# Kernel tuning notes

Hardware: AMD Instinct MI355X
Metric: run time of the kernel (lower is better)

The kernel has to match this reference:

```python
import jax, jax.numpy as jnp
import numpy as np


def setup_inputs() -> dict:
    key = jax.random.key(0)
    k1, k2 = jax.random.split(key)
    x = jax.random.normal(k1, (32, 64, 64, 64), dtype=jnp.float32)  # [B, C, H, W]
    limit = 3 ** 0.5
    embeddings = jax.random.uniform(k2, (64, 512), dtype=jnp.float32,
                                    minval=-limit, maxval=limit)  # [D, K]
    return {"x": x, "embeddings": embeddings}


def reference(x, embeddings):
    B, D, H, W = x.shape
    # NCHW -> NHWC -> [N, D]
    flat_x = jnp.transpose(x, (0, 2, 3, 1)).reshape(-1, D)
    distances = (
        jnp.sum(flat_x ** 2, axis=1, keepdims=True)
        - 2.0 * flat_x @ embeddings
        + jnp.sum(embeddings ** 2, axis=0, keepdims=True)
    )
    encoding_indices = jnp.argmin(distances, axis=1)  # [N]
    # gather codebook rows: embeddings.T is [K, D]
    quantized = embeddings.T[encoding_indices].reshape(B, H, W, D)
    quantized = jnp.transpose(quantized, (0, 3, 1, 2))  # back to NCHW
    commitment_loss = jnp.mean((x - jax.lax.stop_gradient(quantized)) ** 2)
    # straight-through estimator
    quantized_ste = x + jax.lax.stop_gradient(quantized - x)
    return quantized_ste, commitment_loss, encoding_indices.reshape(B, -1)
```

## Files before the change

kernel.cpp:

```cpp
#include <hip/hip_runtime.h>

#define D      64
#define K      512
#define Q_OFF  0
#define L_OFF  8388608
#define I_OFF  8388609

#define WS_ET    0
#define WS_EN    32768
#define WS_ENH   33280
#define WS_PART  33792
#define WS_BH    40960
#define WS_BL    57344

#define SEL_SCALE 16384.0f
#define SEL_BIAS  (160.0f * 16384.0f)

typedef __attribute__((ext_vector_type(8))) short short8;
typedef __attribute__((ext_vector_type(4))) float f32x4;

static __device__ __forceinline__ unsigned short f2bf(float f) {
    unsigned u = __float_as_uint(f);
    u += 0x7fffu + ((u >> 16) & 1u);
    return (unsigned short)(u >> 16);
}
static __device__ __forceinline__ float bf2f(unsigned short h) {
    return __uint_as_float(((unsigned)h) << 16);
}

__device__ __forceinline__ void gload_lds16(const float* g, float* l) {
    __builtin_amdgcn_global_load_lds(
        (const __attribute__((address_space(1))) unsigned int*)g,
        (__attribute__((address_space(3))) unsigned int*)l, 16, 0, 0);
}

__global__ __launch_bounds__(256) void vq_prep(const float* __restrict__ E,
                                               float* __restrict__ ws) {
    int g = blockIdx.x * 256 + threadIdx.x;
    int t = g >> 6, lane = g & 63;
    int col = lane & 15, kg = lane >> 4;
    int code = t * 16 + col;
    short8* bhp = (short8*)(ws + WS_BH);
    short8* blp = (short8*)(ws + WS_BL);
#pragma unroll
    for (int s = 0; s < 2; ++s) {
        short8 h, l;
#pragma unroll
        for (int j = 0; j < 8; ++j) {
            int k = s * 32 + kg * 8 + j;
            float v = -E[k * K + code];
            unsigned short hb = f2bf(v);
            h[j] = (short)hb;
            l[j] = (short)f2bf(v - bf2f(hb));
        }
        bhp[(t * 2 + s) * 64 + lane] = h;
        blp[(t * 2 + s) * 64 + lane] = l;
    }
    if (g < K) {
        float nsq = 0.f;
#pragma unroll 8
        for (int d = 0; d < D; ++d) {
            float v = E[d * K + g];
            ws[WS_ET + g * D + d] = v;
            nsq = fmaf(v, v, nsq);
        }
        ws[WS_EN + g]  = nsq;
        ws[WS_ENH + g] = 0.5f * nsq;
    }
}

__device__ __forceinline__ float dot16(const float* __restrict__ er,
                                       const float* __restrict__ xv) {
    const float4* e4 = (const float4*)er;
    float a0 = 0.f, a1 = 0.f, a2 = 0.f, a3 = 0.f;
#pragma unroll
    for (int q = 0; q < 4; ++q) {
        float4 e = e4[q];
        a0 = fmaf(xv[4*q+0], e.x, a0);
        a1 = fmaf(xv[4*q+1], e.y, a1);
        a2 = fmaf(xv[4*q+2], e.z, a2);
        a3 = fmaf(xv[4*q+3], e.w, a3);
    }
    return (a0 + a1) + (a2 + a3);
}

__global__ __launch_bounds__(128, 8) void vq_fused(const float* __restrict__ x,
                                                   float* __restrict__ ws,
                                                   float* __restrict__ out,
                                                   float* __restrict__ partial) {
    __shared__ float sbuf[2][1024];
    __shared__ unsigned sc[32];
    __shared__ float2 sdot[4][32];
    __shared__ float wsum[2];

    const int tid = threadIdx.x, w = tid >> 6, lane = tid & 63;
    const int col = lane & 15, rowg = lane >> 4;
    const int pixw = blockIdx.x * 32 + w * 16;

    const float* bh    = ws + WS_BH;
    const float* bl    = ws + WS_BL;
    const float* enh_g = ws + WS_ENH;

    gload_lds16(bh + tid * 4, sbuf[0] + tid * 4);
    gload_lds16(bl + tid * 4, sbuf[0] + 512 + tid * 4);

    short8 ah[2], al[2];
    {
        int pix = pixw + col;
        const float* xp = x + ((size_t)(pix >> 12) << 18) + (pix & 4095);
#pragma unroll
        for (int s = 0; s < 2; ++s) {
            short8 h, l;
#pragma unroll
            for (int j = 0; j < 8; ++j) {
                float v = xp[(size_t)(s * 32 + rowg * 8 + j) << 12];
                unsigned short hb = f2bf(v);
                h[j] = (short)hb;
                l[j] = (short)f2bf(v - bf2f(hb));
            }
            ah[s] = h; al[s] = l;
        }
    }

    unsigned m1[4], m2[4];
#pragma unroll
    for (int r = 0; r < 4; ++r) { m1[r] = 0xFFFFFFFFu; m2[r] = 0xFFFFFFFFu; }

    __syncthreads();

    for (int c = 0; c < 32; ++c) {
        if (c + 1 < 32) {
            const float* sh = bh + (c + 1) * 512;
            const float* sl = bl + (c + 1) * 512;
            float* db = sbuf[(c + 1) & 1];
            gload_lds16(sh + tid * 4, db + tid * 4);
            gload_lds16(sl + tid * 4, db + 512 + tid * 4);
        }

        const short8* sb = (const short8*)sbuf[c & 1];
        const float ev = enh_g[c * 16 + col];
        const unsigned codev = (unsigned)(c * 16 + col);

        short8 cbh0 = sb[lane];
        short8 cbh1 = sb[64 + lane];
        short8 cbl0 = sb[128 + lane];
        short8 cbl1 = sb[192 + lane];

        f32x4 acc = { ev, ev, ev, ev };
        __builtin_amdgcn_s_setprio(1);
        acc = __builtin_amdgcn_mfma_f32_16x16x32_bf16(ah[0], cbh0, acc, 0, 0, 0);
        acc = __builtin_amdgcn_mfma_f32_16x16x32_bf16(al[0], cbh0, acc, 0, 0, 0);
        acc = __builtin_amdgcn_mfma_f32_16x16x32_bf16(ah[0], cbl0, acc, 0, 0, 0);
        acc = __builtin_amdgcn_mfma_f32_16x16x32_bf16(ah[1], cbh1, acc, 0, 0, 0);
        acc = __builtin_amdgcn_mfma_f32_16x16x32_bf16(al[1], cbh1, acc, 0, 0, 0);
        acc = __builtin_amdgcn_mfma_f32_16x16x32_bf16(ah[1], cbl1, acc, 0, 0, 0);
        __builtin_amdgcn_s_setprio(0);

#pragma unroll
        for (int r = 0; r < 4; ++r) {
            unsigned p0 = (((unsigned)fmaf(acc[r], SEL_SCALE, SEL_BIAS)) << 9) + codev;
            m2[r] = min(m2[r], max(m1[r], p0));
            m1[r] = min(m1[r], p0);
        }

        __syncthreads();
    }

#pragma unroll
    for (int r = 0; r < 4; ++r) {
        unsigned v1 = m1[r], v2 = m2[r];
#pragma unroll
        for (int m = 1; m < 16; m <<= 1) {
            unsigned o1 = (unsigned)__shfl_xor((int)v1, m, 16);
            unsigned o2 = (unsigned)__shfl_xor((int)v2, m, 16);
            v2 = min(max(v1, o1), min(v2, o2));
            v1 = min(v1, o1);
        }
        if (col == r)
            sc[w * 16 + rowg * 4 + r] = (v1 & 511u) | ((v2 & 511u) << 16);
    }
    __syncthreads();

    const float* ET = ws + WS_ET;
    const float* EN = ws + WS_EN;
    const int pl   = tid & 31;
    const int part = tid >> 5;
    const int n    = blockIdx.x * 32 + pl;
    const int b    = n >> 12;
    const int hw   = n & 4095;

    unsigned pk = sc[pl];
    int c1 = (int)(pk & 0xffffu), c2 = (int)(pk >> 16);

    const float* xp2 = x + ((size_t)b << 18) + ((size_t)part << 16) + hw;
    float xv2[16];
#pragma unroll
    for (int d = 0; d < 16; ++d) xv2[d] = xp2[(size_t)d << 12];

    float dp1 = dot16(ET + (c1 << 6) + part * 16, xv2);
    float dp2 = dot16(ET + (c2 << 6) + part * 16, xv2);
    sdot[part][pl] = make_float2(dp1, dp2);
    __syncthreads();
    float2 q0 = sdot[0][pl], q1 = sdot[1][pl], q2 = sdot[2][pl], q3 = sdot[3][pl];
    float d1 = fmaf(-2.f, (q0.x + q1.x) + (q2.x + q3.x), EN[c1]);
    float d2 = fmaf(-2.f, (q0.y + q1.y) + (q2.y + q3.y), EN[c2]);
    bool sw = (d2 < d1) || (d2 == d1 && c2 < c1);
    int bestk = sw ? c2 : c1;

    if (part == 0) out[I_OFF + n] = (float)bestk;

    const float* qv = ET + (bestk << 6) + part * 16;
    float* op = out + Q_OFF + ((size_t)b << 18) + ((size_t)part << 16) + hw;
    float lsum = 0.f;
#pragma unroll
    for (int d = 0; d < 16; ++d) {
        float qd = qv[d];
        op[(size_t)d << 12] = qd;
        float diff = xv2[d] - qd;
        lsum = fmaf(diff, diff, lsum);
    }

#pragma unroll
    for (int off = 32; off > 0; off >>= 1)
        lsum += __shfl_down(lsum, off, 64);
    if ((tid & 63) == 0) wsum[tid >> 6] = lsum;
    __syncthreads();
    if (tid == 0)
        partial[blockIdx.x] = wsum[0] + wsum[1];
}

__global__ __launch_bounds__(256) void vq_final(const float* __restrict__ partial,
                                                float* __restrict__ out) {
    int t = threadIdx.x;
    float s = 0.f;
#pragma unroll
    for (int i = 0; i < 16; ++i) s += partial[t + 256 * i];
#pragma unroll
    for (int off = 32; off > 0; off >>= 1)
        s += __shfl_down(s, off, 64);
    __shared__ float wsum[4];
    if ((t & 63) == 0) wsum[t >> 6] = s;
    __syncthreads();
    if (t == 0)
        out[L_OFF] = ((wsum[0] + wsum[1]) + (wsum[2] + wsum[3])) * (1.f / 8388608.f);
}

extern "C" void kernel_launch(void* const* d_in, const int* in_sizes, int n_in,
                              void* d_out, int out_size, void* d_ws, size_t ws_size,
                              hipStream_t stream) {
    const float* x = (const float*)d_in[0];
    const float* E = (const float*)d_in[1];
    float* out = (float*)d_out;
    float* ws  = (float*)d_ws;

    hipLaunchKernelGGL(vq_prep,  dim3(8),    dim3(256), 0, stream, E, ws);
    hipLaunchKernelGGL(vq_fused, dim3(4096), dim3(128), 0, stream, x, ws, out, ws + WS_PART);
    hipLaunchKernelGGL(vq_final, dim3(1),    dim3(256), 0, stream, ws + WS_PART, out);
}
```

Before: 61.64 us.

## Keep codebook slices register-resident per wave and loop over pixel tiles

Each of the 8 waves in a 512-thread block now holds a fixed 64-code slice of the bf16 hi/lo codebook in registers. Every wave loops over 16 pixel tiles and computes top-2 candidates for its slice, and the per-slice candidates are merged through shared memory. This removes the per-iteration LDS streaming of the codebook and the block barriers inside the main loop, but each wave now re-reads and re-splits x for every tile, so x is loaded eight times. The grid shrinks to 512 blocks, which lowers occupancy and parallelism, and the final reduction is adjusted to match.

```diff
diff --git a/kernel.cpp b/kernel.cpp
--- a/kernel.cpp
+++ b/kernel.cpp
@@ -26,12 +26,6 @@
 }
 static __device__ __forceinline__ float bf2f(unsigned short h) {
     return __uint_as_float(((unsigned)h) << 16);
-}
-
-__device__ __forceinline__ void gload_lds16(const float* g, float* l) {
-    __builtin_amdgcn_global_load_lds(
-        (const __attribute__((address_space(1))) unsigned int*)g,
-        (__attribute__((address_space(3))) unsigned int*)l, 16, 0, 0);
 }
 
 __global__ __launch_bounds__(256) void vq_prep(const float* __restrict__ E,
@@ -84,157 +78,160 @@
     return (a0 + a1) + (a2 + a3);
 }
 
-__global__ __launch_bounds__(128, 8) void vq_fused(const float* __restrict__ x,
+__global__ __launch_bounds__(512, 2) void vq_fused(const float* __restrict__ x,
                                                    float* __restrict__ ws,
                                                    float* __restrict__ out,
                                                    float* __restrict__ partial) {
-    __shared__ float sbuf[2][1024];
-    __shared__ unsigned sc[32];
-    __shared__ float2 sdot[4][32];
-    __shared__ float wsum[2];
+    __shared__ uint2  scand[16 * 16 * 9];
+    __shared__ float2 sdot[4][128];
+    __shared__ float  wsum8[8];
 
     const int tid = threadIdx.x, w = tid >> 6, lane = tid & 63;
     const int col = lane & 15, rowg = lane >> 4;
-    const int pixw = blockIdx.x * 32 + w * 16;
-
-    const float* bh    = ws + WS_BH;
-    const float* bl    = ws + WS_BL;
-    const float* enh_g = ws + WS_ENH;
-
-    gload_lds16(bh + tid * 4, sbuf[0] + tid * 4);
-    gload_lds16(bl + tid * 4, sbuf[0] + 512 + tid * 4);
-
-    short8 ah[2], al[2];
-    {
-        int pix = pixw + col;
-        const float* xp = x + ((size_t)(pix >> 12) << 18) + (pix & 4095);
+
+    const short8* bhp = (const short8*)(ws + WS_BH);
+    const short8* blp = (const short8*)(ws + WS_BL);
+
+    short8 Bh[4][2], Bl[4][2];
+#pragma unroll
+    for (int nt = 0; nt < 4; ++nt)
 #pragma unroll
         for (int s = 0; s < 2; ++s) {
-            short8 h, l;
-#pragma unroll
-            for (int j = 0; j < 8; ++j) {
-                float v = xp[(size_t)(s * 32 + rowg * 8 + j) << 12];
-                unsigned short hb = f2bf(v);
-                h[j] = (short)hb;
-                l[j] = (short)f2bf(v - bf2f(hb));
+            int t = 4 * w + nt;
+            Bh[nt][s] = bhp[(t * 2 + s) * 64 + lane];
+            Bl[nt][s] = blp[(t * 2 + s) * 64 + lane];
+        }
+    float evc[4]; unsigned codev[4];
+#pragma unroll
+    for (int nt = 0; nt < 4; ++nt) {
+        evc[nt]   = ws[WS_ENH + (4 * w + nt) * 16 + col];
+        codev[nt] = (unsigned)((4 * w + nt) * 16 + col);
+    }
+
+    for (int m = 0; m < 16; ++m) {
+        const int pixw = (blockIdx.x * 16 + m) * 16;
+
+        short8 ah[2], al[2];
+        {
+            int pix = pixw + col;
+            const float* xp = x + ((size_t)(pix >> 12) << 18) + (pix & 4095);
+#pragma unroll
+            for (int s = 0; s < 2; ++s) {
+                short8 h, l;
+#pragma unroll
+                for (int j = 0; j < 8; ++j) {
+                    float v = xp[(size_t)(s * 32 + rowg * 8 + j) << 12];
+                    unsigned short hb = f2bf(v);
+                    h[j] = (short)hb;
+                    l[j] = (short)f2bf(v - bf2f(hb));
+                }
+                ah[s] = h; al[s] = l;
             }
-            ah[s] = h; al[s] = l;
-        }
-    }
-
-    unsigned m1[4], m2[4];
-#pragma unroll
-    for (int r = 0; r < 4; ++r) { m1[r] = 0xFFFFFFFFu; m2[r] = 0xFFFFFFFFu; }
-
-    __syncthreads();
-
-    for (int c = 0; c < 32; ++c) {
-        if (c + 1 < 32) {
-            const float* sh = bh + (c + 1) * 512;
-            const float* sl = bl + (c + 1) * 512;
-            float* db = sbuf[(c + 1) & 1];
-            gload_lds16(sh + tid * 4, db + tid * 4);
-            gload_lds16(sl + tid * 4, db + 512 + tid * 4);
-        }
-
-        const short8* sb = (const short8*)sbuf[c & 1];
-        const float ev = enh_g[c * 16 + col];
-        const unsigned codev = (unsigned)(c * 16 + col);
-
-        short8 cbh0 = sb[lane];
-        short8 cbh1 = sb[64 + lane];
-        short8 cbl0 = sb[128 + lane];
-        short8 cbl1 = sb[192 + lane];
-
-        f32x4 acc = { ev, ev, ev, ev };
-        __builtin_amdgcn_s_setprio(1);
-        acc = __builtin_amdgcn_mfma_f32_16x16x32_bf16(ah[0], cbh0, acc, 0, 0, 0);
-        acc = __builtin_amdgcn_mfma_f32_16x16x32_bf16(al[0], cbh0, acc, 0, 0, 0);
-        acc = __builtin_amdgcn_mfma_f32_16x16x32_bf16(ah[0], cbl0, acc, 0, 0, 0);
-        acc = __builtin_amdgcn_mfma_f32_16x16x32_bf16(ah[1], cbh1, acc, 0, 0, 0);
-        acc = __builtin_amdgcn_mfma_f32_16x16x32_bf16(al[1], cbh1, acc, 0, 0, 0);
-        acc = __builtin_amdgcn_mfma_f32_16x16x32_bf16(ah[1], cbl1, acc, 0, 0, 0);
-        __builtin_amdgcn_s_setprio(0);
+        }
+
+        unsigned m1[4] = {~0u, ~0u, ~0u, ~0u}, m2[4] = {~0u, ~0u, ~0u, ~0u};
+#pragma unroll
+        for (int nt = 0; nt < 4; ++nt) {
+            f32x4 acc = { evc[nt], evc[nt], evc[nt], evc[nt] };
+            __builtin_amdgcn_s_setprio(1);
+            acc = __builtin_amdgcn_mfma_f32_16x16x32_bf16(ah[0], Bh[nt][0], acc, 0, 0, 0);
+            acc = __builtin_amdgcn_mfma_f32_16x16x32_bf16(al[0], Bh[nt][0], acc, 0, 0, 0);
+            acc = __builtin_amdgcn_mfma_f32_16x16x32_bf16(ah[0], Bl[nt][0], acc, 0, 0, 0);
+            acc = __builtin_amdgcn_mfma_f32_16x16x32_bf16(ah[1], Bh[nt][1], acc, 0, 0, 0);
+            acc = __builtin_amdgcn_mfma_f32_16x16x32_bf16(al[1], Bh[nt][1], acc, 0, 0, 0);
+            acc = __builtin_amdgcn_mfma_f32_16x16x32_bf16(ah[1], Bl[nt][1], acc, 0, 0, 0);
+            __builtin_amdgcn_s_setprio(0);
+#pragma unroll
+            for (int r = 0; r < 4; ++r) {
+                unsigned p = (((unsigned)fmaf(acc[r], SEL_SCALE, SEL_BIAS)) << 9) + codev[nt];
+                m2[r] = min(m2[r], max(m1[r], p));
+                m1[r] = min(m1[r], p);
+            }
+        }
 
 #pragma unroll
         for (int r = 0; r < 4; ++r) {
-            unsigned p0 = (((unsigned)fmaf(acc[r], SEL_SCALE, SEL_BIAS)) << 9) + codev;
-            m2[r] = min(m2[r], max(m1[r], p0));
-            m1[r] = min(m1[r], p0);
-        }
-
-        __syncthreads();
-    }
-
-#pragma unroll
-    for (int r = 0; r < 4; ++r) {
-        unsigned v1 = m1[r], v2 = m2[r];
-#pragma unroll
-        for (int m = 1; m < 16; m <<= 1) {
-            unsigned o1 = (unsigned)__shfl_xor((int)v1, m, 16);
-            unsigned o2 = (unsigned)__shfl_xor((int)v2, m, 16);
-            v2 = min(max(v1, o1), min(v2, o2));
-            v1 = min(v1, o1);
-        }
-        if (col == r)
-            sc[w * 16 + rowg * 4 + r] = (v1 & 511u) | ((v2 & 511u) << 16);
+            unsigned v1 = m1[r], v2 = m2[r];
+#pragma unroll
+            for (int mm = 1; mm < 16; mm <<= 1) {
+                unsigned o1 = (unsigned)__shfl_xor((int)v1, mm, 16);
+                unsigned o2 = (unsigned)__shfl_xor((int)v2, mm, 16);
+                v2 = min(max(v1, o1), min(v2, o2));
+                v1 = min(v1, o1);
+            }
+            if (col == r)
+                scand[(m * 16 + rowg * 4 + r) * 9 + w] = make_uint2(v1, v2);
+        }
     }
     __syncthreads();
 
     const float* ET = ws + WS_ET;
     const float* EN = ws + WS_EN;
-    const int pl   = tid & 31;
-    const int part = tid >> 5;
-    const int n    = blockIdx.x * 32 + pl;
-    const int b    = n >> 12;
-    const int hw   = n & 4095;
-
-    unsigned pk = sc[pl];
-    int c1 = (int)(pk & 0xffffu), c2 = (int)(pk >> 16);
-
-    const float* xp2 = x + ((size_t)b << 18) + ((size_t)part << 16) + hw;
-    float xv2[16];
-#pragma unroll
-    for (int d = 0; d < 16; ++d) xv2[d] = xp2[(size_t)d << 12];
-
-    float dp1 = dot16(ET + (c1 << 6) + part * 16, xv2);
-    float dp2 = dot16(ET + (c2 << 6) + part * 16, xv2);
-    sdot[part][pl] = make_float2(dp1, dp2);
-    __syncthreads();
-    float2 q0 = sdot[0][pl], q1 = sdot[1][pl], q2 = sdot[2][pl], q3 = sdot[3][pl];
-    float d1 = fmaf(-2.f, (q0.x + q1.x) + (q2.x + q3.x), EN[c1]);
-    float d2 = fmaf(-2.f, (q0.y + q1.y) + (q2.y + q3.y), EN[c2]);
-    bool sw = (d2 < d1) || (d2 == d1 && c2 < c1);
-    int bestk = sw ? c2 : c1;
-
-    if (part == 0) out[I_OFF + n] = (float)bestk;
-
-    const float* qv = ET + (bestk << 6) + part * 16;
-    float* op = out + Q_OFF + ((size_t)b << 18) + ((size_t)part << 16) + hw;
+    const int pl   = tid & 127;
+    const int part = tid >> 7;
     float lsum = 0.f;
-#pragma unroll
-    for (int d = 0; d < 16; ++d) {
-        float qd = qv[d];
-        op[(size_t)d << 12] = qd;
-        float diff = xv2[d] - qd;
-        lsum = fmaf(diff, diff, lsum);
+
+#pragma unroll
+    for (int pass = 0; pass < 2; ++pass) {
+        const int pxb = pass * 128 + pl;
+        const int n   = blockIdx.x * 256 + pxb;
+        const int b   = n >> 12;
+        const int hw  = n & 4095;
+
+        unsigned a = ~0u, bb = ~0u;
+#pragma unroll
+        for (int ww = 0; ww < 8; ++ww) {
+            uint2 cp = scand[pxb * 9 + ww];
+            bb = min(max(a, cp.x), bb); a = min(a, cp.x);
+            bb = min(bb, cp.y);
+        }
+        int c1 = (int)(a & 511u), c2 = (int)(bb & 511u);
+
+        const float* xp2 = x + ((size_t)b << 18) + ((size_t)part << 16) + hw;
+        float xv2[16];
+#pragma unroll
+        for (int d = 0; d < 16; ++d) xv2[d] = xp2[(size_t)d << 12];
+
+        float dp1 = dot16(ET + (c1 << 6) + part * 16, xv2);
+        float dp2 = dot16(ET + (c2 << 6) + part * 16, xv2);
+        sdot[part][pl] = make_float2(dp1, dp2);
+        __syncthreads();
+        float2 q0 = sdot[0][pl], q1 = sdot[1][pl], q2 = sdot[2][pl], q3 = sdot[3][pl];
+        float d1 = fmaf(-2.f, (q0.x + q1.x) + (q2.x + q3.x), EN[c1]);
+        float d2 = fmaf(-2.f, (q0.y + q1.y) + (q2.y + q3.y), EN[c2]);
+        bool sw = (d2 < d1) || (d2 == d1 && c2 < c1);
+        int bestk = sw ? c2 : c1;
+
+        if (part == 0) out[I_OFF + n] = (float)bestk;
+
+        const float* qv = ET + (bestk << 6) + part * 16;
+        float* op = out + Q_OFF + ((size_t)b << 18) + ((size_t)part << 16) + hw;
+#pragma unroll
+        for (int d = 0; d < 16; ++d) {
+            float qd = qv[d];
+            op[(size_t)d << 12] = qd;
+            float diff = xv2[d] - qd;
+            lsum = fmaf(diff, diff, lsum);
+        }
+        __syncthreads();
     }
 
 #pragma unroll
     for (int off = 32; off > 0; off >>= 1)
         lsum += __shfl_down(lsum, off, 64);
-    if ((tid & 63) == 0) wsum[tid >> 6] = lsum;
+    if ((tid & 63) == 0) wsum8[tid >> 6] = lsum;
     __syncthreads();
-    if (tid == 0)
-        partial[blockIdx.x] = wsum[0] + wsum[1];
+    if (tid == 0) {
+        float s = ((wsum8[0] + wsum8[1]) + (wsum8[2] + wsum8[3]))
+                + ((wsum8[4] + wsum8[5]) + (wsum8[6] + wsum8[7]));
+        partial[blockIdx.x] = s;
+    }
 }
 
 __global__ __launch_bounds__(256) void vq_final(const float* __restrict__ partial,
                                                 float* __restrict__ out) {
     int t = threadIdx.x;
-    float s = 0.f;
-#pragma unroll
-    for (int i = 0; i < 16; ++i) s += partial[t + 256 * i];
+    float s = partial[t] + partial[t + 256];
 #pragma unroll
     for (int off = 32; off > 0; off >>= 1)
         s += __shfl_down(s, off, 64);
@@ -253,7 +250,7 @@
     float* out = (float*)d_out;
     float* ws  = (float*)d_ws;
 
-    hipLaunchKernelGGL(vq_prep,  dim3(8),    dim3(256), 0, stream, E, ws);
-    hipLaunchKernelGGL(vq_fused, dim3(4096), dim3(128), 0, stream, x, ws, out, ws + WS_PART);
-    hipLaunchKernelGGL(vq_final, dim3(1),    dim3(256), 0, stream, ws + WS_PART, out);
-}
+    hipLaunchKernelGGL(vq_prep,  dim3(8),   dim3(256), 0, stream, E, ws);
+    hipLaunchKernelGGL(vq_fused, dim3(512), dim3(512), 0, stream, x, ws, out, ws + WS_PART);
+    hipLaunchKernelGGL(vq_final, dim3(1),   dim3(256), 0, stream, ws + WS_PART, out);
+}
```

Result: slower. 87.81 us (+42.5%).
